# Performance work log

Hardware: AMD Instinct MI355X
Metric: run time of the kernel (lower is better)

The kernel has to match this reference:

```python
import jax, jax.numpy as jnp
import numpy as np

N = 50000; E = 800000; F_IN = 165; HID = 32; H1 = 8; H3 = 4; OUT = 2
D1 = H1 * HID  # 256
D3 = H3 * HID  # 128
BN_EPS = 1e-5


def _gat_conv(x, edge_index, W, a_s, a_d, b, heads, add_self_loops):
    n = x.shape[0]
    if add_self_loops:
        loops = jnp.arange(n, dtype=edge_index.dtype)
        edge_index = jnp.concatenate([edge_index, jnp.stack([loops, loops])], axis=1)
    src, dst = edge_index[0], edge_index[1]
    h = (x @ W).reshape(n, heads, -1)                      # [N, H, D]
    a_src = jnp.sum(h * a_s, axis=-1)                      # [N, H]
    a_dst = jnp.sum(h * a_d, axis=-1)                      # [N, H]
    e = jax.nn.leaky_relu(a_src[src] + a_dst[dst], 0.2)    # [E, H] per-edge logits
    m = jax.ops.segment_max(e, dst, num_segments=n)        # segment-softmax over incoming edges
    ex = jnp.exp(e - m[dst])
    den = jax.ops.segment_sum(ex, dst, num_segments=n)
    alpha = ex / (den[dst] + 1e-16)                        # PyG softmax eps
    out = jax.ops.segment_sum(h[src] * alpha[:, :, None], dst, num_segments=n)
    return out.reshape(n, -1) + b                          # concat heads + bias


def _bn(x, g, b, mean, var):  # eval-mode BatchNorm1d
    return (x - mean) * jax.lax.rsqrt(var + BN_EPS) * g + b


def setup_inputs() -> dict:
    key = jax.random.key(0)
    ks = jax.random.split(key, 24)
    rn = lambda i, shape, s=0.05: jax.random.normal(ks[i], shape, dtype=jnp.float32) * s
    d = {}
    d["x"] = jax.random.normal(ks[0], (N, F_IN), dtype=jnp.float32)
    d["edge_index"] = jax.random.randint(ks[1], (2, E), 0, N, dtype=jnp.int32)
    d["W1"] = rn(2, (F_IN, D1)); d["a1s"] = rn(3, (H1, HID)); d["a1d"] = rn(4, (H1, HID))
    d["b1"] = jnp.zeros((D1,), jnp.float32)
    d["g1"] = jnp.ones((D1,), jnp.float32); d["be1"] = jnp.zeros((D1,), jnp.float32)
    d["m1"] = rn(5, (D1,)); d["v1"] = jax.random.uniform(ks[6], (D1,), minval=0.5, maxval=1.5)
    d["W2"] = rn(7, (D1, D1)); d["a2s"] = rn(8, (H1, HID)); d["a2d"] = rn(9, (H1, HID))
    d["b2"] = jnp.zeros((D1,), jnp.float32)
    d["g2"] = jnp.ones((D1,), jnp.float32); d["be2"] = jnp.zeros((D1,), jnp.float32)
    d["m2"] = rn(10, (D1,)); d["v2"] = jax.random.uniform(ks[11], (D1,), minval=0.5, maxval=1.5)
    d["W3"] = rn(12, (D1, D3)); d["a3s"] = rn(13, (H3, HID)); d["a3d"] = rn(14, (H3, HID))
    d["b3"] = jnp.zeros((D3,), jnp.float32)
    d["fcW"] = rn(15, (D3, OUT)); d["fcb"] = jnp.zeros((OUT,), jnp.float32)
    d["skW"] = rn(16, (F_IN, D3)); d["skb"] = jnp.zeros((D3,), jnp.float32)
    d["temp"] = jnp.array(1.0, jnp.float32)
    return d


def reference(x, edge_index, W1, a1s, a1d, b1, g1, be1, m1, v1,
              W2, a2s, a2d, b2, g2, be2, m2, v2,
              W3, a3s, a3d, b3, fcW, fcb, skW, skb, temp):
    x_init = x @ skW + skb                                   # skip Linear
    h = jax.nn.elu(_bn(_gat_conv(x, edge_index, W1, a1s, a1d, b1, H1, False), g1, be1, m1, v1))
    h = jax.nn.elu(_bn(_gat_conv(h, edge_index, W2, a2s, a2d, b2, H1, True), g2, be2, m2, v2) + h)
    h = _gat_conv(h * temp, edge_index, W3, a3s, a3d, b3, H3, True)
    return jax.nn.log_softmax((h + x_init) @ fcW + fcb, axis=1)
```

## Files before the change

kernel.cpp:

```cpp
#include <hip/hip_runtime.h>
#include <hip/hip_bf16.h>
#include <math.h>

#define N_NODES 50000
#define MP      50048
#define N_EDGES 800000
#define F_IN    165
#define KPAD1   192
#define D1      256
#define D3      128
#define CAP     64

typedef __attribute__((ext_vector_type(8))) short short8;
typedef __attribute__((ext_vector_type(4))) float floatx4;
typedef __attribute__((ext_vector_type(2))) float floatx2;

__device__ __forceinline__ float bflo(unsigned u) { return __uint_as_float(u << 16); }
__device__ __forceinline__ float bfhi(unsigned u) { return __uint_as_float(u & 0xffff0000u); }

__device__ __forceinline__ void fma8p(floatx2* a, float wgt, const uint4& v) {
    floatx2 w2; w2.x = wgt; w2.y = wgt;
    floatx2 p;
    p.x = bflo(v.x); p.y = bfhi(v.x); a[0] += w2 * p;
    p.x = bflo(v.y); p.y = bfhi(v.y); a[1] += w2 * p;
    p.x = bflo(v.z); p.y = bfhi(v.z); a[2] += w2 * p;
    p.x = bflo(v.w); p.y = bfhi(v.w); a[3] += w2 * p;
}

#if defined(__has_builtin)
#if __has_builtin(__builtin_amdgcn_global_load_lds)
#define HAS_GLL 1
#endif
#endif

__device__ __forceinline__ void gload16(const void* g, void* lds) {
#ifdef HAS_GLL
    __builtin_amdgcn_global_load_lds(
        (const __attribute__((address_space(1))) unsigned*)g,
        (__attribute__((address_space(3))) unsigned*)lds, 16, 0, 0);
#else
    *(int4*)lds = *(const int4*)g;
#endif
}

__global__ void prep_hist(const int* __restrict__ ei, int* __restrict__ deg,
                          const float* __restrict__ x, __hip_bfloat16* __restrict__ xb,
                          const float* __restrict__ W1, const float* __restrict__ skW,
                          const float* __restrict__ a1s, const float* __restrict__ a1d,
                          __hip_bfloat16* __restrict__ Bt1,
                          const float* __restrict__ W2,
                          const float* __restrict__ a2s, const float* __restrict__ a2d,
                          __hip_bfloat16* __restrict__ Bt2,
                          const float* __restrict__ W3,
                          const float* __restrict__ a3s, const float* __restrict__ a3d,
                          __hip_bfloat16* __restrict__ Bt3)
{
    long long gidx = (long long)blockIdx.x * 256 + threadIdx.x;
    if (gidx < N_EDGES) {
        atomicAdd(&deg[ei[N_EDGES + gidx]], 1);
        return;
    }
    long long idx = gidx - N_EDGES;
    const long long S0 = (long long)MP * KPAD1;
    const long long S1 = S0 + 256 * KPAD1;
    const long long S2 = S1 + 128 * KPAD1;
    const long long S3 = S2 + 16 * KPAD1;
    const long long S4 = S3 + 256 * D1;
    const long long S5 = S4 + 16 * D1;
    const long long S6 = S5 + 128 * D1;
    const long long S7 = S6 + 8 * D1;
    if (idx < S0) {
        const int m = idx / KPAD1, k = idx - (long long)m * KPAD1;
        xb[idx] = __float2bfloat16((k < F_IN && m < N_NODES) ? x[(size_t)m * F_IN + k] : 0.f);
    } else if (idx < S1) {
        const long long i = idx - S0;
        const int n = i / KPAD1, k = i - (long long)n * KPAD1;
        Bt1[(size_t)n * KPAD1 + k] = __float2bfloat16((k < F_IN) ? W1[(size_t)k * D1 + n] : 0.f);
    } else if (idx < S2) {
        const long long i = idx - S1;
        const int n = i / KPAD1, k = i - (long long)n * KPAD1;
        Bt1[(size_t)(256 + n) * KPAD1 + k] =
            __float2bfloat16((k < F_IN) ? skW[(size_t)k * D3 + n] : 0.f);
    } else if (idx < S3) {
        const long long i = idx - S2;
        const int r = i / KPAD1, k = i - (long long)r * KPAD1;
        const int hh = r & 7;
        const float* av = (r < 8) ? a1s : a1d;
        float s = 0.f;
        if (k < F_IN)
#pragma unroll
            for (int d = 0; d < 32; ++d) s += W1[(size_t)k * D1 + hh * 32 + d] * av[hh * 32 + d];
        Bt1[(size_t)(384 + r) * KPAD1 + k] = __float2bfloat16(s);
    } else if (idx < S4) {
        const long long i = idx - S3;
        const int n = i / D1, k = i - (long long)n * D1;
        Bt2[(size_t)n * D1 + k] = __float2bfloat16(W2[(size_t)k * D1 + n]);
    } else if (idx < S5) {
        const long long i = idx - S4;
        const int r = i / D1, k = i - (long long)r * D1;
        const int hh = r & 7;
        const float* av = (r < 8) ? a2s : a2d;
        float s = 0.f;
#pragma unroll
        for (int d = 0; d < 32; ++d) s += W2[(size_t)k * D1 + hh * 32 + d] * av[hh * 32 + d];
        Bt2[(size_t)(256 + r) * D1 + k] = __float2bfloat16(s);
    } else if (idx < S6) {
        const long long i = idx - S5;
        const int n = i / D1, k = i - (long long)n * D1;
        Bt3[(size_t)n * D1 + k] = __float2bfloat16(W3[(size_t)k * D3 + n]);
    } else if (idx < S7) {
        const long long i = idx - S6;
        const int r = i / D1, k = i - (long long)r * D1;
        const int hh = r & 3;
        const float* av = (r < 4) ? a3s : a3d;
        float s = 0.f;
#pragma unroll
        for (int d = 0; d < 32; ++d) s += W3[(size_t)k * D3 + hh * 32 + d] * av[hh * 32 + d];
        Bt3[(size_t)(128 + r) * D1 + k] = __float2bfloat16(s);
    }
}

__global__ __launch_bounds__(256, 4) void gemm_bf16(
    const __hip_bfloat16* __restrict__ A, const __hip_bfloat16* __restrict__ Bt,
    const float* __restrict__ alphap,
    __hip_bfloat16* __restrict__ Cb, int Dh,
    __hip_bfloat16* __restrict__ Cx, const float* __restrict__ biasx, int Dx,
    float* __restrict__ asrc, float* __restrict__ adst, int H,
    int M, int Ka)
{
    __shared__ short As[128 * 32];
    __shared__ short Bs[128 * 32];
    const int t  = threadIdx.x;
    const int m0 = blockIdx.x * 128;
    const int n0 = blockIdx.y * 128;
    const int w  = t >> 6, l = t & 63;
    const int wy = w >> 1, wx = w & 1;
    const int lm = l & 15, quad = l >> 4;
    const float alpha = alphap ? alphap[0] : 1.f;
    const int NNlive = Dh + Dx + 2 * H;

    floatx4 acc[4][4] = {};

    const int ch0 = w * 128 + l;
    const int ch1 = ch0 + 64;
    const int r0a = ch0 >> 2, k0a = (ch0 & 3) * 8;
    const int r1a = ch1 >> 2, k1a = (ch1 & 3) * 8;

    for (int k0 = 0; k0 < Ka; k0 += 32) {
        gload16(A  + (size_t)(m0 + r0a) * Ka + k0 + k0a, &As[ch0 * 8]);
        gload16(A  + (size_t)(m0 + r1a) * Ka + k0 + k1a, &As[ch1 * 8]);
        gload16(Bt + (size_t)(n0 + r0a) * Ka + k0 + k0a, &Bs[ch0 * 8]);
        gload16(Bt + (size_t)(n0 + r1a) * Ka + k0 + k1a, &Bs[ch1 * 8]);
        __syncthreads();

        short8 af[4], bf[4];
#pragma unroll
        for (int i = 0; i < 4; ++i) {
            af[i] = *(const short8*)&As[(wy * 64 + i * 16 + lm) * 32 + quad * 8];
            bf[i] = *(const short8*)&Bs[(wx * 64 + i * 16 + lm) * 32 + quad * 8];
        }
#pragma unroll
        for (int mi = 0; mi < 4; ++mi)
#pragma unroll
            for (int ni = 0; ni < 4; ++ni)
                acc[mi][ni] = __builtin_amdgcn_mfma_f32_16x16x32_bf16(
                    af[mi], bf[ni], acc[mi][ni], 0, 0, 0);
        __syncthreads();
    }

#pragma unroll
    for (int mi = 0; mi < 4; ++mi) {
#pragma unroll
        for (int r = 0; r < 4; ++r) {
            const int gm = m0 + wy * 64 + mi * 16 + quad * 4 + r;
            if (gm >= M) continue;
#pragma unroll
            for (int ni = 0; ni < 4; ++ni) {
                const int gn = n0 + wx * 64 + ni * 16 + lm;
                if (gn >= NNlive) continue;
                const float v = acc[mi][ni][r] * alpha;
                if (gn < Dh) {
                    Cb[(size_t)gm * Dh + gn] = __float2bfloat16(v);
                } else if (gn < Dh + Dx) {
                    Cx[(size_t)gm * Dx + gn - Dh] = __float2bfloat16(v + biasx[gn - Dh]);
                } else {
                    const int c = gn - Dh - Dx;
                    if (c < H) asrc[(size_t)gm * H + c] = v;
                    else       adst[(size_t)gm * H + c - H] = v;
                }
            }
        }
    }
}

__global__ __launch_bounds__(1024) void scan_rowptr(const int* __restrict__ deg,
                                                    int* __restrict__ rowptr, int n)
{
    __shared__ int sums[1024];
    const int tid = threadIdx.x;
    const int chunk = (n + 1023) / 1024;
    const int lo = tid * chunk;
    const int hi = min(lo + chunk, n);
    int s = 0;
    for (int i = lo; i < hi; ++i) s += deg[i];
    sums[tid] = s;
    __syncthreads();
    for (int off = 1; off < 1024; off <<= 1) {
        int t = 0;
        if (tid >= off) t = sums[tid - off];
        __syncthreads();
        if (tid >= off) sums[tid] += t;
        __syncthreads();
    }
    int run = sums[tid] - s;
    for (int i = lo; i < hi; ++i) { rowptr[i] = run; run += deg[i]; }
    if (lo < n && hi == n) rowptr[n] = run;
}

__global__ void csr_fill(const int* __restrict__ ei, const int* __restrict__ rowptr,
                         int* __restrict__ cursor, int* __restrict__ csr_src, int E)
{
    const int e = blockIdx.x * blockDim.x + threadIdx.x;
    if (e >= E) return;
    const int dst = ei[E + e];
    const int pos = rowptr[dst] + atomicAdd(&cursor[dst], 1);
    csr_src[pos] = ei[e];
}

template <int HSH, int D, int POST>
__global__ __launch_bounds__(256) void gat_gather_v9(
    const __hip_bfloat16* __restrict__ h, const float* __restrict__ asrc,
    const float* __restrict__ adst, const int* __restrict__ rowptr,
    const int* __restrict__ csr_src, int selfloop,
    const float* __restrict__ bias, const float* __restrict__ g,
    const float* __restrict__ be, const float* __restrict__ mean,
    const float* __restrict__ var, const __hip_bfloat16* __restrict__ residB,
    const float* __restrict__ fcW, const float* __restrict__ fcb,
    float* __restrict__ outF, __hip_bfloat16* __restrict__ outB)
{
    constexpr int H    = 1 << HSH;
    constexpr int LPE  = D / 8;
    constexpr int EPW  = 64 / LPE;
    constexpr int SUBS = 64 >> HSH;
    constexpr int MAXJ = CAP / SUBS;

    const int w = threadIdx.x >> 6, l = threadIdx.x & 63;
    const int node = blockIdx.x * 4 + w;

    __shared__ float sW[4][CAP * H];
    __shared__ int   sSrc[4][CAP];

    const int r0  = rowptr[node];
    const int deg = rowptr[node + 1] - r0;
    const int tot = min(deg + selfloop, CAP);

    const int hh  = l & (H - 1);
    const int sub = l >> HSH;
    const float ad = adst[node * H + hh];

    float ex[MAXJ];
    float sum = 0.f;
    {
        int nj = 0;
        for (int e = sub; e < tot; e += SUBS, ++nj) {
            const int s = (e < deg) ? csr_src[r0 + e] : node;
            if (hh == 0) sSrc[w][e] = s;
            float v = asrc[s * H + hh] + ad;
            v = v > 0.f ? v : 0.2f * v;
            ex[nj] = __expf(v);
            sum += ex[nj];
        }
    }
#pragma unroll
    for (int off = H; off < 64; off <<= 1) sum += __shfl_xor(sum, off);
    const float rs = 1.f / (sum + 1e-16f);
    {
        int nj = 0;
        for (int e = sub; e < tot; e += SUBS, ++nj)
            sW[w][e * H + hh] = ex[nj] * rs;
    }

    const int sw   = l / LPE;
    const int lo   = l % LPE;
    const int dimb = lo * 8;
    const int hh2  = dimb >> 5;
    floatx2 a0[4] = {}, a1[4] = {};

    for (int e = sw; e < tot; e += 2 * EPW) {
        const int e2  = e + EPW;
        const bool v2 = e2 < tot;
        const int sa = sSrc[w][e];
        const int sb = v2 ? sSrc[w][e2] : node;
        const float wa = sW[w][e * H + hh2];
        const float wb = v2 ? sW[w][e2 * H + hh2] : 0.f;
        const uint4 qa = *(const uint4*)&h[(size_t)sa * D + dimb];
        const uint4 qb = *(const uint4*)&h[(size_t)sb * D + dimb];
        fma8p(a0, wa, qa);
        fma8p(a1, wb, qb);
    }
    float acc[8];
#pragma unroll
    for (int v = 0; v < 4; ++v) {
        const floatx2 s2v = a0[v] + a1[v];
        acc[v * 2] = s2v.x; acc[v * 2 + 1] = s2v.y;
    }
#pragma unroll
    for (int off = LPE; off < 64; off <<= 1)
#pragma unroll
        for (int v = 0; v < 8; ++v) acc[v] += __shfl_xor(acc[v], off);

    if (POST == 3) {
        float v0 = 0.f, v1 = 0.f;
        if (l < LPE) {
            const uint4 rv = *(const uint4*)&residB[(size_t)node * D + dimb];
            const float rr[8] = {bflo(rv.x), bfhi(rv.x), bflo(rv.y), bfhi(rv.y),
                                 bflo(rv.z), bfhi(rv.z), bflo(rv.w), bfhi(rv.w)};
#pragma unroll
            for (int v = 0; v < 8; ++v) {
                const float val = acc[v] + bias[dimb + v] + rr[v];
                v0 += val * fcW[(dimb + v) * 2 + 0];
                v1 += val * fcW[(dimb + v) * 2 + 1];
            }
        }
#pragma unroll
        for (int off = 1; off < LPE; off <<= 1) {
            v0 += __shfl_xor(v0, off);
            v1 += __shfl_xor(v1, off);
        }
        if (l == 0) {
            const float l0 = v0 + fcb[0], l1 = v1 + fcb[1];
            const float m2 = fmaxf(l0, l1);
            const float lse = m2 + logf(__expf(l0 - m2) + __expf(l1 - m2));
            outF[node * 2 + 0] = l0 - lse;
            outF[node * 2 + 1] = l1 - lse;
        }
    } else {
        if (l < LPE) {
            float rr[8] = {};
            if (POST == 2) {
                const uint4 rv = *(const uint4*)&residB[(size_t)node * D + dimb];
                rr[0] = bflo(rv.x); rr[1] = bfhi(rv.x);
                rr[2] = bflo(rv.y); rr[3] = bfhi(rv.y);
                rr[4] = bflo(rv.z); rr[5] = bfhi(rv.z);
                rr[6] = bflo(rv.w); rr[7] = bfhi(rv.w);
            }
            __hip_bfloat16 rb[8];
#pragma unroll
            for (int v = 0; v < 8; ++v) {
                const int f = dimb + v;
                float vv = acc[v] + bias[f];
                vv = (vv - mean[f]) * rsqrtf(var[f] + 1e-5f) * g[f] + be[f];
                if (POST == 2) vv += rr[v];
                vv = vv > 0.f ? vv : (__expf(vv) - 1.f);
                rb[v] = __float2bfloat16(vv);
            }
            *(uint4*)&outB[(size_t)node * D + dimb] = *(uint4*)&rb[0];
        }
    }
}

extern "C" void kernel_launch(void* const* d_in, const int* in_sizes, int n_in,
                              void* d_out, int out_size, void* d_ws, size_t ws_size,
                              hipStream_t stream)
{
    const float* x    = (const float*)d_in[0];
    const int*   ei   = (const int*)  d_in[1];
    const float* W1   = (const float*)d_in[2];
    const float* a1s  = (const float*)d_in[3];
    const float* a1d  = (const float*)d_in[4];
    const float* b1   = (const float*)d_in[5];
    const float* g1   = (const float*)d_in[6];
    const float* be1  = (const float*)d_in[7];
    const float* m1   = (const float*)d_in[8];
    const float* v1   = (const float*)d_in[9];
    const float* W2   = (const float*)d_in[10];
    const float* a2s  = (const float*)d_in[11];
    const float* a2d  = (const float*)d_in[12];
    const float* b2   = (const float*)d_in[13];
    const float* g2   = (const float*)d_in[14];
    const float* be2  = (const float*)d_in[15];
    const float* m2   = (const float*)d_in[16];
    const float* v2   = (const float*)d_in[17];
    const float* W3   = (const float*)d_in[18];
    const float* a3s  = (const float*)d_in[19];
    const float* a3d  = (const float*)d_in[20];
    const float* b3   = (const float*)d_in[21];
    const float* fcW  = (const float*)d_in[22];
    const float* fcb  = (const float*)d_in[23];
    const float* skW  = (const float*)d_in[24];
    const float* skb  = (const float*)d_in[25];
    const float* temp = (const float*)d_in[26];

    float* out = (float*)d_out;

    const int N = N_NODES, E = N_EDGES;

    float* ws = (float*)d_ws;
    size_t o = 0;
    float* asrc  = ws + o;  o += (size_t)N * 8;
    float* adst  = ws + o;  o += (size_t)N * 8;
    int* rowptr  = (int*)(ws + o);  o += N + 1;
    o = (o + 3) & ~(size_t)3;
    int* csr_src = (int*)(ws + o);  o += E;
    o = (o + 3) & ~(size_t)3;
    __hip_bfloat16* xb     = (__hip_bfloat16*)(ws + o); o += (size_t)MP * KPAD1 / 2;
    __hip_bfloat16* bufCb  = (__hip_bfloat16*)(ws + o); o += (size_t)MP * D1 / 2;
    __hip_bfloat16* hb     = (__hip_bfloat16*)(ws + o); o += (size_t)N * D1 / 2;
    __hip_bfloat16* xinitB = (__hip_bfloat16*)(ws + o); o += (size_t)N * D3 / 2;
    __hip_bfloat16* Bt1    = (__hip_bfloat16*)(ws + o); o += (size_t)512 * KPAD1 / 2;
    __hip_bfloat16* Bt2    = (__hip_bfloat16*)(ws + o); o += (size_t)384 * D1 / 2;
    __hip_bfloat16* Bt3    = (__hip_bfloat16*)(ws + o); o += (size_t)256 * D1 / 2;
    int* deg    = (int*)hb;
    int* cursor = deg + N;

    const int MT128 = MP / 128;

    hipMemsetAsync(deg, 0, (size_t)2 * N * sizeof(int), stream);
    {
        const long long tote = (long long)E + (long long)MP * KPAD1 +
                               (256 + 128 + 16) * (long long)KPAD1 +
                               (256 + 16 + 128 + 8) * (long long)D1;
        prep_hist<<<(tote + 255) / 256, 256, 0, stream>>>(
            ei, deg, x, xb, W1, skW, a1s, a1d, Bt1, W2, a2s, a2d, Bt2, W3, a3s, a3d, Bt3);
    }
    scan_rowptr<<<1, 1024, 0, stream>>>(deg, rowptr, N);
    csr_fill<<<(E + 255) / 256, 256, 0, stream>>>(ei, rowptr, cursor, csr_src, E);

    gemm_bf16<<<dim3(MT128, 4), 256, 0, stream>>>(xb, Bt1, nullptr,
                                                  hb, D1, xinitB, skb, D3,
                                                  asrc, adst, 8, N, KPAD1);
    gat_gather_v9<3, D1, 1><<<N / 4, 256, 0, stream>>>(hb, asrc, adst, rowptr, csr_src, 0,
                                                       b1, g1, be1, m1, v1, nullptr, nullptr, nullptr,
                                                       nullptr, bufCb);

    gemm_bf16<<<dim3(MT128, 3), 256, 0, stream>>>(bufCb, Bt2, nullptr,
                                                  hb, D1, nullptr, nullptr, 0,
                                                  asrc, adst, 8, N, D1);
    gat_gather_v9<3, D1, 2><<<N / 4, 256, 0, stream>>>(hb, asrc, adst, rowptr, csr_src, 1,
                                                       b2, g2, be2, m2, v2, bufCb, nullptr, nullptr,
                                                       nullptr, bufCb);

    gemm_bf16<<<dim3(MT128, 2), 256, 0, stream>>>(bufCb, Bt3, temp,
                                                  hb, D3, nullptr, nullptr, 0,
                                                  asrc, adst, 4, N, D1);
    gat_gather_v9<2, D3, 3><<<N / 4, 256, 0, stream>>>(hb, asrc, adst, rowptr, csr_src, 1,
                                                       b3, nullptr, nullptr, nullptr, nullptr, xinitB,
                                                       fcW, fcb, out, nullptr);

    (void)in_sizes; (void)n_in; (void)out_size; (void)ws_size;
}
```

Before: 604.3 us.

## Double-buffer GEMM shared tiles and parallelize rowptr scan across blocks

The bf16 GEMM now uses two shared-memory buffers so the next K-tile's global loads are issued before the current tile's MFMAs, and one barrier per iteration is dropped. This is meant to hide global load latency behind matrix math, at the cost of doubling the LDS footprint, which may reduce occupancy. The single-block serial rowptr scan is replaced by a three-kernel parallel scan (block scans, a partial scan, then an add), removing a long single-block serial pass in exchange for two extra launches. The scan_part kernel assumes at most 128 blocks, which holds for N=50000 with 512-thread blocks.

```diff
diff --git a/kernel.cpp b/kernel.cpp
--- a/kernel.cpp
+++ b/kernel.cpp
@@ -10,6 +10,7 @@
 #define D1      256
 #define D3      128
 #define CAP     64
+#define SCB     512
 
 typedef __attribute__((ext_vector_type(8))) short short8;
 typedef __attribute__((ext_vector_type(4))) float floatx4;
@@ -128,8 +129,8 @@
     float* __restrict__ asrc, float* __restrict__ adst, int H,
     int M, int Ka)
 {
-    __shared__ short As[128 * 32];
-    __shared__ short Bs[128 * 32];
+    __shared__ short As[2][128 * 32];
+    __shared__ short Bs[2][128 * 32];
     const int t  = threadIdx.x;
     const int m0 = blockIdx.x * 128;
     const int n0 = blockIdx.y * 128;
@@ -138,6 +139,7 @@
     const int lm = l & 15, quad = l >> 4;
     const float alpha = alphap ? alphap[0] : 1.f;
     const int NNlive = Dh + Dx + 2 * H;
+    const int KT = Ka >> 5;
 
     floatx4 acc[4][4] = {};
 
@@ -146,18 +148,28 @@
     const int r0a = ch0 >> 2, k0a = (ch0 & 3) * 8;
     const int r1a = ch1 >> 2, k1a = (ch1 & 3) * 8;
 
-    for (int k0 = 0; k0 < Ka; k0 += 32) {
-        gload16(A  + (size_t)(m0 + r0a) * Ka + k0 + k0a, &As[ch0 * 8]);
-        gload16(A  + (size_t)(m0 + r1a) * Ka + k0 + k1a, &As[ch1 * 8]);
-        gload16(Bt + (size_t)(n0 + r0a) * Ka + k0 + k0a, &Bs[ch0 * 8]);
-        gload16(Bt + (size_t)(n0 + r1a) * Ka + k0 + k1a, &Bs[ch1 * 8]);
+    gload16(A  + (size_t)(m0 + r0a) * Ka + k0a, &As[0][ch0 * 8]);
+    gload16(A  + (size_t)(m0 + r1a) * Ka + k1a, &As[0][ch1 * 8]);
+    gload16(Bt + (size_t)(n0 + r0a) * Ka + k0a, &Bs[0][ch0 * 8]);
+    gload16(Bt + (size_t)(n0 + r1a) * Ka + k1a, &Bs[0][ch1 * 8]);
+
+    for (int kt = 0; kt < KT; ++kt) {
         __syncthreads();
+        const int cur = kt & 1;
+        if (kt + 1 < KT) {
+            const int nxt = cur ^ 1;
+            const int k0 = (kt + 1) << 5;
+            gload16(A  + (size_t)(m0 + r0a) * Ka + k0 + k0a, &As[nxt][ch0 * 8]);
+            gload16(A  + (size_t)(m0 + r1a) * Ka + k0 + k1a, &As[nxt][ch1 * 8]);
+            gload16(Bt + (size_t)(n0 + r0a) * Ka + k0 + k0a, &Bs[nxt][ch0 * 8]);
+            gload16(Bt + (size_t)(n0 + r1a) * Ka + k0 + k1a, &Bs[nxt][ch1 * 8]);
+        }
 
         short8 af[4], bf[4];
 #pragma unroll
         for (int i = 0; i < 4; ++i) {
-            af[i] = *(const short8*)&As[(wy * 64 + i * 16 + lm) * 32 + quad * 8];
-            bf[i] = *(const short8*)&Bs[(wx * 64 + i * 16 + lm) * 32 + quad * 8];
+            af[i] = *(const short8*)&As[cur][(wy * 64 + i * 16 + lm) * 32 + quad * 8];
+            bf[i] = *(const short8*)&Bs[cur][(wx * 64 + i * 16 + lm) * 32 + quad * 8];
         }
 #pragma unroll
         for (int mi = 0; mi < 4; ++mi)
@@ -165,7 +177,6 @@
             for (int ni = 0; ni < 4; ++ni)
                 acc[mi][ni] = __builtin_amdgcn_mfma_f32_16x16x32_bf16(
                     af[mi], bf[ni], acc[mi][ni], 0, 0, 0);
-        __syncthreads();
     }
 
 #pragma unroll
@@ -193,28 +204,48 @@
     }
 }
 
-__global__ __launch_bounds__(1024) void scan_rowptr(const int* __restrict__ deg,
-                                                    int* __restrict__ rowptr, int n)
-{
-    __shared__ int sums[1024];
-    const int tid = threadIdx.x;
-    const int chunk = (n + 1023) / 1024;
-    const int lo = tid * chunk;
-    const int hi = min(lo + chunk, n);
-    int s = 0;
-    for (int i = lo; i < hi; ++i) s += deg[i];
-    sums[tid] = s;
+__global__ __launch_bounds__(SCB) void scan_blk(const int* __restrict__ deg,
+                                                int* __restrict__ rowptr,
+                                                int* __restrict__ part, int n)
+{
+    __shared__ int s[SCB];
+    const int i = blockIdx.x * SCB + threadIdx.x;
+    const int v = (i < n) ? deg[i] : 0;
+    s[threadIdx.x] = v;
     __syncthreads();
-    for (int off = 1; off < 1024; off <<= 1) {
-        int t = 0;
-        if (tid >= off) t = sums[tid - off];
+    for (int off = 1; off < SCB; off <<= 1) {
+        int tv = 0;
+        if (threadIdx.x >= off) tv = s[threadIdx.x - off];
         __syncthreads();
-        if (tid >= off) sums[tid] += t;
+        s[threadIdx.x] += tv;
         __syncthreads();
     }
-    int run = sums[tid] - s;
-    for (int i = lo; i < hi; ++i) { rowptr[i] = run; run += deg[i]; }
-    if (lo < n && hi == n) rowptr[n] = run;
+    if (i < n) rowptr[i] = s[threadIdx.x] - v;
+    if (threadIdx.x == SCB - 1) part[blockIdx.x] = s[SCB - 1];
+}
+
+__global__ __launch_bounds__(128) void scan_part(int* __restrict__ part, int nb)
+{
+    __shared__ int s[128];
+    const int v = (threadIdx.x < nb) ? part[threadIdx.x] : 0;
+    s[threadIdx.x] = v;
+    __syncthreads();
+    for (int off = 1; off < 128; off <<= 1) {
+        int tv = 0;
+        if (threadIdx.x >= off) tv = s[threadIdx.x - off];
+        __syncthreads();
+        s[threadIdx.x] += tv;
+        __syncthreads();
+    }
+    if (threadIdx.x < nb) part[threadIdx.x] = s[threadIdx.x] - v;
+}
+
+__global__ __launch_bounds__(SCB) void scan_add(int* __restrict__ rowptr,
+                                                const int* __restrict__ part, int n)
+{
+    const int i = blockIdx.x * SCB + threadIdx.x;
+    if (i < n) rowptr[i] += part[blockIdx.x];
+    if (i == 0) rowptr[n] = N_EDGES;
 }
 
 __global__ void csr_fill(const int* __restrict__ ei, const int* __restrict__ rowptr,
@@ -394,6 +425,7 @@
     float* out = (float*)d_out;
 
     const int N = N_NODES, E = N_EDGES;
+    const int NB = (N + SCB - 1) / SCB;
 
     float* ws = (float*)d_ws;
     size_t o = 0;
@@ -403,6 +435,7 @@
     o = (o + 3) & ~(size_t)3;
     int* csr_src = (int*)(ws + o);  o += E;
     o = (o + 3) & ~(size_t)3;
+    int* part    = (int*)(ws + o);  o += 128;
     __hip_bfloat16* xb     = (__hip_bfloat16*)(ws + o); o += (size_t)MP * KPAD1 / 2;
     __hip_bfloat16* bufCb  = (__hip_bfloat16*)(ws + o); o += (size_t)MP * D1 / 2;
     __hip_bfloat16* hb     = (__hip_bfloat16*)(ws + o); o += (size_t)N * D1 / 2;
@@ -423,7 +456,9 @@
         prep_hist<<<(tote + 255) / 256, 256, 0, stream>>>(
             ei, deg, x, xb, W1, skW, a1s, a1d, Bt1, W2, a2s, a2d, Bt2, W3, a3s, a3d, Bt3);
     }
-    scan_rowptr<<<1, 1024, 0, stream>>>(deg, rowptr, N);
+    scan_blk<<<NB, SCB, 0, stream>>>(deg, rowptr, part, N);
+    scan_part<<<1, 128, 0, stream>>>(part, NB);
+    scan_add<<<NB, SCB, 0, stream>>>(rowptr, part, N);
     csr_fill<<<(E + 255) / 256, 256, 0, stream>>>(ei, rowptr, cursor, csr_src, E);
 
     gemm_bf16<<<dim3(MT128, 4), 256, 0, stream>>>(xb, Bt1, nullptr,
```

After: 534.0 us, median of 2. -11.6%, faster.
